# Kernel tuning notes

Measured on AMD Instinct MI355X. Metric: run time of the kernel, lower is better.

## Reference

```python
import jax, jax.numpy as jnp
import numpy as np

N_LAYERS = 3
N_HEADS = 8
N_HIDDEN = 16  # hidden_dim // n_heads
HIDDEN = 128
SLOPE = 0.2


def setup_inputs() -> dict:
    key = jax.random.key(0)
    ks = jax.random.split(key, 7)
    B, N, Din, Dh = 4, 512, 2, HIDDEN
    node_features = jax.random.normal(ks[0], (B, N, Din), dtype=jnp.float32)
    adj = jax.random.randint(ks[1], (B, N, N), 0, 2).astype(jnp.int32)
    adj = jnp.maximum(adj, jnp.eye(N, dtype=jnp.int32)[None])  # self loops -> no empty softmax rows
    s = 1.0 / np.sqrt(Dh)
    W_in = jax.random.normal(ks[2], (Din, Dh), dtype=jnp.float32) * (1.0 / np.sqrt(Din))
    W_l = jax.random.normal(ks[3], (N_LAYERS, Dh, N_HEADS * N_HIDDEN), dtype=jnp.float32) * s
    W_r = jax.random.normal(ks[4], (N_LAYERS, Dh, N_HEADS * N_HIDDEN), dtype=jnp.float32) * s
    attn_a = jax.random.normal(ks[5], (N_LAYERS, N_HIDDEN), dtype=jnp.float32) * (1.0 / np.sqrt(N_HIDDEN))
    W_out = jax.random.normal(ks[6], (Dh, 1), dtype=jnp.float32) * s
    return {"node_features": node_features, "adj": adj, "W_in": W_in,
            "W_l": W_l, "W_r": W_r, "attn_a": attn_a, "W_out": W_out}


def _gatv2_layer(h, adj, Wl, Wr, a):
    # h: [B,N,Dh]; adj: [B,N,N] int; Wl/Wr: [Dh, H*F]; a: [F]
    B, N, _ = h.shape
    g_l = (h @ Wl).reshape(B, N, N_HEADS, N_HIDDEN)
    g_r = (h @ Wr).reshape(B, N, N_HEADS, N_HIDDEN)
    # torch: g_sum[b,i,j] = g_l[b,j] + g_r[b,i]  (repeat vs repeat_interleave)
    g_sum = g_r[:, :, None, :, :] + g_l[:, None, :, :, :]  # [B,N,N,H,F]
    e = jnp.einsum('bijhf,f->bijh', jax.nn.leaky_relu(g_sum, SLOPE), a)  # [B,N,N,H]
    e = jnp.where(adj[..., None] == 0, -jnp.inf, e)
    att = jax.nn.softmax(e, axis=2)  # softmax over neighbors j
    out = jnp.einsum('bijh,bjhf->bihf', att, g_r)  # aggregate g_r (per source)
    return out.reshape(B, N, N_HEADS * N_HIDDEN)


def reference(node_features, adj, W_in, W_l, W_r, attn_a, W_out):
    h = node_features @ W_in  # [B,N,128]
    for i in range(N_LAYERS):
        h = _gatv2_layer(h, adj, W_l[i], W_r[i], attn_a[i])
    return h @ W_out  # [B,N,1]
```

## Files before the change

kernel.cpp:

```cpp
#include <hip/hip_runtime.h>
#include <cstdint>
#include <math.h>

#define NB 4
#define NN 512
#define DH 128
#define NHEADS 8
#define NHID 16
#define SLOPE 0.2f
#define ITILE 64
#define SENTINEL -1e30f

__global__ __launch_bounds__(256) void pack_adj_kernel(
    const int* __restrict__ adj, uint32_t* __restrict__ adjb)
{
    const int t   = threadIdx.x;
    const int row = blockIdx.x * 16 + (t >> 4);
    const int w   = t & 15;
    const int4* p = (const int4*)(adj + (size_t)row * NN + w * 32);
    uint32_t m = 0;
#pragma unroll
    for (int c = 0; c < 8; ++c) {
        const int4 v = p[c];
        m |= (v.x != 0 ? 1u : 0u) << (c * 4 + 0);
        m |= (v.y != 0 ? 1u : 0u) << (c * 4 + 1);
        m |= (v.z != 0 ? 1u : 0u) << (c * 4 + 2);
        m |= (v.w != 0 ? 1u : 0u) << (c * 4 + 3);
    }
    adjb[(size_t)row * 16 + w] = m;
}

__global__ __launch_bounds__(256) void proj_kernel(
    const float* __restrict__ h, const float* __restrict__ X,
    const float* __restrict__ Win,
    const float* __restrict__ Wl, const float* __restrict__ Wr,
    float* __restrict__ gl, float* __restrict__ gr)
{
    __shared__ __align__(16) float s_h[8][DH];
    const int bn0 = blockIdx.x * 8;
    const int b   = bn0 >> 9;
    const int n0  = bn0 & 511;
    const int t   = threadIdx.x;

    if (X) {
        if (t < DH) {
            const float w0 = Win[t], w1 = Win[DH + t];
#pragma unroll
            for (int r = 0; r < 8; ++r) {
                const float x0 = X[(bn0 + r) * 2 + 0];
                const float x1 = X[(bn0 + r) * 2 + 1];
                s_h[r][t] = x0 * w0 + x1 * w1;
            }
        }
    } else {
        for (int idx = t; idx < 8 * DH; idx += 256)
            s_h[idx >> 7][idx & 127] = h[(size_t)bn0 * DH + idx];
    }
    __syncthreads();

    const float* W = (t < DH) ? Wl : Wr;
    float*       g = (t < DH) ? gl : gr;
    const int f128 = t & 127;
    float acc[8] = {};
    for (int k = 0; k < DH; k += 4) {
        const float w0 = W[(k + 0) * DH + f128];
        const float w1 = W[(k + 1) * DH + f128];
        const float w2 = W[(k + 2) * DH + f128];
        const float w3 = W[(k + 3) * DH + f128];
#pragma unroll
        for (int r = 0; r < 8; ++r) {
            const float4 hv = *(const float4*)&s_h[r][k];
            acc[r] += hv.x * w0 + hv.y * w1 + hv.z * w2 + hv.w * w3;
        }
    }
    const int hh = f128 >> 4, f = f128 & 15;
    float* dst = g + ((size_t)(b * NHEADS + hh) * NN + n0) * NHID + f;
#pragma unroll
    for (int r = 0; r < 8; ++r)
        dst[r * NHID] = acc[r];
}

__global__ __launch_bounds__(512, 1) void attn_kernel(
    const float* __restrict__ gl, const float* __restrict__ gr,
    const uint32_t* __restrict__ adjb, const float* __restrict__ a_vec,
    float* __restrict__ h_out,
    const float* __restrict__ Wout, float* __restrict__ out)
{
    __shared__ __align__(16) float smem[19616];
    float* s_gl  = smem;
    float* s_gr  = smem + 8192;
    float* s_acc = smem;
    float* s_dgl = smem + 16384;
    float* s_dgr = smem + 16896;
    float* s_m   = smem + 17408;
    float* s_l   = smem + 18448;
    float* s_M   = smem + 19488;
    float* s_inv = smem + 19552;

    const int blk = blockIdx.x;
    const int it  = blk & 7;
    const int bh  = blk >> 3;
    const int b   = bh >> 3;
    const int hh  = bh & 7;
    const int i0  = it * ITILE;
    const int t   = threadIdx.x;
    const int il  = t & 31;
    const int js  = t >> 5;
    const int r0  = i0 + il;
    const int r1  = r0 + 32;

    const float4* pgl = (const float4*)(gl + (size_t)bh * NN * NHID);
    const float4* pgr = (const float4*)(gr + (size_t)bh * NN * NHID);
    float4 rl[4], rr[4];
#pragma unroll
    for (int k = 0; k < 4; ++k) { rl[k] = pgl[k * 512 + t]; rr[k] = pgr[k * 512 + t]; }

    const uint32_t mask0 = adjb[((size_t)(b * NN + r0)) * 16 + js];
    const uint32_t mask1 = adjb[((size_t)(b * NN + r1)) * 16 + js];

    float gri0[16], gri1[16];
#pragma unroll
    for (int q = 0; q < 4; ++q) {
        const float4 v0 = pgr[r0 * 4 + q];
        const float4 v1 = pgr[r1 * 4 + q];
        gri0[4*q+0] = v0.x; gri0[4*q+1] = v0.y; gri0[4*q+2] = v0.z; gri0[4*q+3] = v0.w;
        gri1[4*q+0] = v1.x; gri1[4*q+1] = v1.y; gri1[4*q+2] = v1.z; gri1[4*q+3] = v1.w;
    }

    float a[16];
#pragma unroll
    for (int q = 0; q < 4; ++q) {
        const float4 v = ((const float4*)a_vec)[q];
        a[4*q+0] = v.x; a[4*q+1] = v.y; a[4*q+2] = v.z; a[4*q+3] = v.w;
    }

    {
        float4* dl = (float4*)s_gl;
        float4* dr = (float4*)s_gr;
#pragma unroll
        for (int k = 0; k < 4; ++k) { dl[k * 512 + t] = rl[k]; dr[k * 512 + t] = rr[k]; }
    }

    {
        const float4 aq = ((const float4*)a_vec)[t & 3];
#pragma unroll
        for (int k = 0; k < 4; ++k) {
            float pl = rl[k].x * aq.x + rl[k].y * aq.y + rl[k].z * aq.z + rl[k].w * aq.w;
            float pr = rr[k].x * aq.x + rr[k].y * aq.y + rr[k].z * aq.z + rr[k].w * aq.w;
            pl += __shfl_xor(pl, 1); pl += __shfl_xor(pl, 2);
            pr += __shfl_xor(pr, 1); pr += __shfl_xor(pr, 2);
            if ((t & 3) == 0) {
                const int row = k * 128 + (t >> 2);
                s_dgl[row] = pl;
                s_dgr[row] = pr;
            }
        }
    }
    __syncthreads();

    const float c0 = 0.6f * s_dgr[r0];
    const float c1 = 0.6f * s_dgr[r1];
    const int jbase = js * 32;
    float sc0[32], sc1[32];
#pragma unroll
    for (int jj = 0; jj < 32; ++jj) {
        const int j = jbase + jj;
        const float4* pg = (const float4*)(s_gl + j * NHID);
        const float dj = s_dgl[j];
        float s0 = 0.f, s1 = 0.f;
#pragma unroll
        for (int q = 0; q < 4; ++q) {
            const float4 g = pg[q];
            float v;
            v = g.x + gri0[4*q+0]; s0 = fmaf(a[4*q+0], fabsf(v), s0);
            v = g.y + gri0[4*q+1]; s0 = fmaf(a[4*q+1], fabsf(v), s0);
            v = g.z + gri0[4*q+2]; s0 = fmaf(a[4*q+2], fabsf(v), s0);
            v = g.w + gri0[4*q+3]; s0 = fmaf(a[4*q+3], fabsf(v), s0);
            v = g.x + gri1[4*q+0]; s1 = fmaf(a[4*q+0], fabsf(v), s1);
            v = g.y + gri1[4*q+1]; s1 = fmaf(a[4*q+1], fabsf(v), s1);
            v = g.z + gri1[4*q+2]; s1 = fmaf(a[4*q+2], fabsf(v), s1);
            v = g.w + gri1[4*q+3]; s1 = fmaf(a[4*q+3], fabsf(v), s1);
        }
        const float b0 = fmaf(0.6f, dj, c0);
        const float b1 = fmaf(0.6f, dj, c1);
        sc0[jj] = ((mask0 >> jj) & 1u) ? fmaf(0.4f, s0, b0) : SENTINEL;
        sc1[jj] = ((mask1 >> jj) & 1u) ? fmaf(0.4f, s1, b1) : SENTINEL;
    }

    float m0 = sc0[0], m1 = sc1[0];
#pragma unroll
    for (int jj = 1; jj < 32; ++jj) { m0 = fmaxf(m0, sc0[jj]); m1 = fmaxf(m1, sc1[jj]); }
    float l0 = 0.f, l1 = 0.f;
#pragma unroll
    for (int jj = 0; jj < 32; ++jj) {
        sc0[jj] = __expf(sc0[jj] - m0); l0 += sc0[jj];
        sc1[jj] = __expf(sc1[jj] - m1); l1 += sc1[jj];
    }
    s_m[js * 65 + il]      = m0;
    s_m[js * 65 + il + 32] = m1;
    s_l[js * 65 + il]      = l0;
    s_l[js * 65 + il + 32] = l1;

    float acc0[16], acc1[16];
#pragma unroll
    for (int f = 0; f < 16; ++f) { acc0[f] = 0.f; acc1[f] = 0.f; }
#pragma unroll
    for (int jj = 0; jj < 32; ++jj) {
        const float4* pg = (const float4*)(s_gr + (jbase + jj) * NHID);
        const float p0 = sc0[jj], p1 = sc1[jj];
#pragma unroll
        for (int q = 0; q < 4; ++q) {
            const float4 g = pg[q];
            acc0[4*q+0] = fmaf(p0, g.x, acc0[4*q+0]);
            acc0[4*q+1] = fmaf(p0, g.y, acc0[4*q+1]);
            acc0[4*q+2] = fmaf(p0, g.z, acc0[4*q+2]);
            acc0[4*q+3] = fmaf(p0, g.w, acc0[4*q+3]);
            acc1[4*q+0] = fmaf(p1, g.x, acc1[4*q+0]);
            acc1[4*q+1] = fmaf(p1, g.y, acc1[4*q+1]);
            acc1[4*q+2] = fmaf(p1, g.z, acc1[4*q+2]);
            acc1[4*q+3] = fmaf(p1, g.w, acc1[4*q+3]);
        }
    }
    __syncthreads();

    if (t < 64) {
        float M = SENTINEL;
#pragma unroll
        for (int k = 0; k < 16; ++k) M = fmaxf(M, s_m[k * 65 + t]);
        float L = 0.f;
#pragma unroll
        for (int k = 0; k < 16; ++k) L += s_l[k * 65 + t] * __expf(s_m[k * 65 + t] - M);
        s_M[t]   = M;
        s_inv[t] = 1.f / L;
    }
    __syncthreads();

    {
        const float k0 = __expf(m0 - s_M[il])      * s_inv[il];
        const float k1 = __expf(m1 - s_M[il + 32]) * s_inv[il + 32];
        const int swz = il & 3;
        float* base_a = s_acc + js * 1024;
#pragma unroll
        for (int q = 0; q < 4; ++q) {
            float4 v0, v1;
            v0.x = acc0[4*q+0] * k0; v0.y = acc0[4*q+1] * k0;
            v0.z = acc0[4*q+2] * k0; v0.w = acc0[4*q+3] * k0;
            v1.x = acc1[4*q+0] * k1; v1.y = acc1[4*q+1] * k1;
            v1.z = acc1[4*q+2] * k1; v1.w = acc1[4*q+3] * k1;
            *(float4*)(base_a + il * 16        + 4 * (q ^ swz)) = v0;
            *(float4*)(base_a + (il + 32) * 16 + 4 * (q ^ swz)) = v1;
        }
    }
    __syncthreads();

    {
        const int i  = t >> 4;
        const int f  = t & 15;
        const int e  = f & 3, qf = f >> 2;
#pragma unroll
        for (int r = 0; r < 2; ++r) {
            const int lr = i + r * 32;
            const int w  = lr * 16 + 4 * (qf ^ (lr & 3)) + e;
            float o = 0.f;
#pragma unroll
            for (int k = 0; k < 16; ++k) o += s_acc[k * 1024 + w];
            const int grow = i0 + lr;
            if (Wout) {
                float v = o * Wout[hh * NHID + f];
#pragma unroll
                for (int off = 8; off; off >>= 1) v += __shfl_xor(v, off);
                if (f == 0) atomicAdd(out + b * NN + grow, v);
            } else {
                h_out[((size_t)(b * NN + grow)) * DH + hh * NHID + f] = o;
            }
        }
    }
}

extern "C" void kernel_launch(void* const* d_in, const int* in_sizes, int n_in,
                              void* d_out, int out_size, void* d_ws, size_t ws_size,
                              hipStream_t stream) {
    const float* X    = (const float*)d_in[0];
    const int*   adj  = (const int*)  d_in[1];
    const float* Win  = (const float*)d_in[2];
    const float* Wl   = (const float*)d_in[3];
    const float* Wr   = (const float*)d_in[4];
    const float* Aa   = (const float*)d_in[5];
    const float* Wout = (const float*)d_in[6];
    float* out = (float*)d_out;

    float*    ws   = (float*)d_ws;
    float*    h    = ws;
    float*    gl   = ws + 262144;
    float*    gr   = ws + 524288;
    uint32_t* adjb = (uint32_t*)(ws + 786432);

    pack_adj_kernel<<<NB * NN / 16, 256, 0, stream>>>(adj, adjb);
    hipMemsetAsync(out, 0, (size_t)out_size * sizeof(float), stream);

    for (int l = 0; l < 3; ++l) {
        proj_kernel<<<NB * NN / 8, 256, 0, stream>>>(
            h, (l == 0) ? X : nullptr, Win,
            Wl + (size_t)l * DH * DH, Wr + (size_t)l * DH * DH, gl, gr);
        const bool last = (l == 2);
        attn_kernel<<<NB * NHEADS * (NN / ITILE), 512, 0, stream>>>(
            gl, gr, adjb, Aa + l * NHID, h,
            last ? Wout : nullptr, out);
    }
}
```

Measured before the change: 163.0 us.

## Fuse projection, adjacency packing and memset into per-layer attention kernel

Merges the adjacency bit-packing, the input/weight projection and the output zeroing into a single per-layer attention kernel. Each block recomputes the per-head g_l/g_r projections for all 512 nodes straight into shared memory, so the separate projection kernel and its global round-trip go away. The launch count drops from eight to three. In exchange, every one of the 8 i-tile blocks per (batch, head) redundantly recomputes the same 512x16x2 projection. Shared memory use also grows, and the g arrays switch to a strided float4 layout.

New measurement: 170.5 us. +4.6%, slower.

```diff
diff --git a/kernel.cpp b/kernel.cpp
--- a/kernel.cpp
+++ b/kernel.cpp
@@ -7,95 +7,31 @@
 #define DH 128
 #define NHEADS 8
 #define NHID 16
-#define SLOPE 0.2f
 #define ITILE 64
 #define SENTINEL -1e30f
 
-__global__ __launch_bounds__(256) void pack_adj_kernel(
-    const int* __restrict__ adj, uint32_t* __restrict__ adjb)
+__global__ __launch_bounds__(512, 1) void gat_layer(
+    const int lay,
+    const float* __restrict__ X, const float* __restrict__ hin,
+    float* __restrict__ hout,
+    const float* __restrict__ Win,
+    const float* __restrict__ WlL, const float* __restrict__ WrL,
+    const float* __restrict__ a_vec, const float* __restrict__ Wout,
+    float* __restrict__ out, uint32_t* __restrict__ adjb,
+    const int* __restrict__ adj)
 {
-    const int t   = threadIdx.x;
-    const int row = blockIdx.x * 16 + (t >> 4);
-    const int w   = t & 15;
-    const int4* p = (const int4*)(adj + (size_t)row * NN + w * 32);
-    uint32_t m = 0;
-#pragma unroll
-    for (int c = 0; c < 8; ++c) {
-        const int4 v = p[c];
-        m |= (v.x != 0 ? 1u : 0u) << (c * 4 + 0);
-        m |= (v.y != 0 ? 1u : 0u) << (c * 4 + 1);
-        m |= (v.z != 0 ? 1u : 0u) << (c * 4 + 2);
-        m |= (v.w != 0 ? 1u : 0u) << (c * 4 + 3);
-    }
-    adjb[(size_t)row * 16 + w] = m;
-}
-
-__global__ __launch_bounds__(256) void proj_kernel(
-    const float* __restrict__ h, const float* __restrict__ X,
-    const float* __restrict__ Win,
-    const float* __restrict__ Wl, const float* __restrict__ Wr,
-    float* __restrict__ gl, float* __restrict__ gr)
-{
-    __shared__ __align__(16) float s_h[8][DH];
-    const int bn0 = blockIdx.x * 8;
-    const int b   = bn0 >> 9;
-    const int n0  = bn0 & 511;
-    const int t   = threadIdx.x;
-
-    if (X) {
-        if (t < DH) {
-            const float w0 = Win[t], w1 = Win[DH + t];
-#pragma unroll
-            for (int r = 0; r < 8; ++r) {
-                const float x0 = X[(bn0 + r) * 2 + 0];
-                const float x1 = X[(bn0 + r) * 2 + 1];
-                s_h[r][t] = x0 * w0 + x1 * w1;
-            }
-        }
-    } else {
-        for (int idx = t; idx < 8 * DH; idx += 256)
-            s_h[idx >> 7][idx & 127] = h[(size_t)bn0 * DH + idx];
-    }
-    __syncthreads();
-
-    const float* W = (t < DH) ? Wl : Wr;
-    float*       g = (t < DH) ? gl : gr;
-    const int f128 = t & 127;
-    float acc[8] = {};
-    for (int k = 0; k < DH; k += 4) {
-        const float w0 = W[(k + 0) * DH + f128];
-        const float w1 = W[(k + 1) * DH + f128];
-        const float w2 = W[(k + 2) * DH + f128];
-        const float w3 = W[(k + 3) * DH + f128];
-#pragma unroll
-        for (int r = 0; r < 8; ++r) {
-            const float4 hv = *(const float4*)&s_h[r][k];
-            acc[r] += hv.x * w0 + hv.y * w1 + hv.z * w2 + hv.w * w3;
-        }
-    }
-    const int hh = f128 >> 4, f = f128 & 15;
-    float* dst = g + ((size_t)(b * NHEADS + hh) * NN + n0) * NHID + f;
-#pragma unroll
-    for (int r = 0; r < 8; ++r)
-        dst[r * NHID] = acc[r];
-}
-
-__global__ __launch_bounds__(512, 1) void attn_kernel(
-    const float* __restrict__ gl, const float* __restrict__ gr,
-    const uint32_t* __restrict__ adjb, const float* __restrict__ a_vec,
-    float* __restrict__ h_out,
-    const float* __restrict__ Wout, float* __restrict__ out)
-{
-    __shared__ __align__(16) float smem[19616];
-    float* s_gl  = smem;
-    float* s_gr  = smem + 8192;
-    float* s_acc = smem;
-    float* s_dgl = smem + 16384;
-    float* s_dgr = smem + 16896;
-    float* s_m   = smem + 17408;
-    float* s_l   = smem + 18448;
-    float* s_M   = smem + 19488;
-    float* s_inv = smem + 19552;
+    __shared__ __align__(16) float smem[23968];
+    float* s_W   = smem;
+    float* s_acc = smem + 4096;
+    float* s_Win = smem + 20480;
+    float* s_dgl = smem + 20736;
+    float* s_dgr = smem + 21248;
+    float* s_m   = smem + 21760;
+    float* s_l   = smem + 22800;
+    float* s_M   = smem + 23840;
+    float* s_inv = smem + 23904;
+    float4* Sgl  = (float4*)(smem + 4096);
+    float4* Sgr  = (float4*)(smem + 12288);
 
     const int blk = blockIdx.x;
     const int it  = blk & 7;
@@ -109,22 +45,11 @@
     const int r0  = i0 + il;
     const int r1  = r0 + 32;
 
-    const float4* pgl = (const float4*)(gl + (size_t)bh * NN * NHID);
-    const float4* pgr = (const float4*)(gr + (size_t)bh * NN * NHID);
-    float4 rl[4], rr[4];
-#pragma unroll
-    for (int k = 0; k < 4; ++k) { rl[k] = pgl[k * 512 + t]; rr[k] = pgr[k * 512 + t]; }
-
-    const uint32_t mask0 = adjb[((size_t)(b * NN + r0)) * 16 + js];
-    const uint32_t mask1 = adjb[((size_t)(b * NN + r1)) * 16 + js];
-
-    float gri0[16], gri1[16];
-#pragma unroll
-    for (int q = 0; q < 4; ++q) {
-        const float4 v0 = pgr[r0 * 4 + q];
-        const float4 v1 = pgr[r1 * 4 + q];
-        gri0[4*q+0] = v0.x; gri0[4*q+1] = v0.y; gri0[4*q+2] = v0.z; gri0[4*q+3] = v0.w;
-        gri1[4*q+0] = v1.x; gri1[4*q+1] = v1.y; gri1[4*q+2] = v1.z; gri1[4*q+3] = v1.w;
+    {
+        const int sk = t >> 2, sq = (t & 3) * 4;
+        *(float4*)&s_W[sk * 32 + sq]      = *(const float4*)&WlL[sk * DH + hh * NHID + sq];
+        *(float4*)&s_W[sk * 32 + 16 + sq] = *(const float4*)&WrL[sk * DH + hh * NHID + sq];
+        if (lay == 0 && t < 64) ((float4*)s_Win)[t] = ((const float4*)Win)[t];
     }
 
     float a[16];
@@ -134,29 +59,106 @@
         a[4*q+0] = v.x; a[4*q+1] = v.y; a[4*q+2] = v.z; a[4*q+3] = v.w;
     }
 
-    {
-        float4* dl = (float4*)s_gl;
-        float4* dr = (float4*)s_gr;
-#pragma unroll
-        for (int k = 0; k < 4; ++k) { dl[k * 512 + t] = rl[k]; dr[k * 512 + t] = rr[k]; }
-    }
-
-    {
-        const float4 aq = ((const float4*)a_vec)[t & 3];
-#pragma unroll
-        for (int k = 0; k < 4; ++k) {
-            float pl = rl[k].x * aq.x + rl[k].y * aq.y + rl[k].z * aq.z + rl[k].w * aq.w;
-            float pr = rr[k].x * aq.x + rr[k].y * aq.y + rr[k].z * aq.z + rr[k].w * aq.w;
-            pl += __shfl_xor(pl, 1); pl += __shfl_xor(pl, 2);
-            pr += __shfl_xor(pr, 1); pr += __shfl_xor(pr, 2);
-            if ((t & 3) == 0) {
-                const int row = k * 128 + (t >> 2);
-                s_dgl[row] = pl;
-                s_dgr[row] = pr;
+    uint32_t mask0, mask1;
+    if (lay == 0) {
+        const int4* p0 = (const int4*)(adj + ((size_t)(b * NN + r0)) * NN + js * 32);
+        const int4* p1 = (const int4*)(adj + ((size_t)(b * NN + r1)) * NN + js * 32);
+        uint32_t m0 = 0, m1 = 0;
+#pragma unroll
+        for (int c = 0; c < 8; ++c) {
+            const int4 v0 = p0[c], v1 = p1[c];
+            m0 |= (v0.x != 0 ? 1u : 0u) << (c * 4 + 0);
+            m0 |= (v0.y != 0 ? 1u : 0u) << (c * 4 + 1);
+            m0 |= (v0.z != 0 ? 1u : 0u) << (c * 4 + 2);
+            m0 |= (v0.w != 0 ? 1u : 0u) << (c * 4 + 3);
+            m1 |= (v1.x != 0 ? 1u : 0u) << (c * 4 + 0);
+            m1 |= (v1.y != 0 ? 1u : 0u) << (c * 4 + 1);
+            m1 |= (v1.z != 0 ? 1u : 0u) << (c * 4 + 2);
+            m1 |= (v1.w != 0 ? 1u : 0u) << (c * 4 + 3);
+        }
+        mask0 = m0; mask1 = m1;
+        adjb[((size_t)(b * NN + r0)) * 16 + js] = m0;
+        adjb[((size_t)(b * NN + r1)) * 16 + js] = m1;
+    } else {
+        mask0 = adjb[((size_t)(b * NN + r0)) * 16 + js];
+        mask1 = adjb[((size_t)(b * NN + r1)) * 16 + js];
+    }
+    __syncthreads();
+
+    float4 agl[4], agr[4];
+#pragma unroll
+    for (int q = 0; q < 4; ++q) {
+        agl[q].x = 0.f; agl[q].y = 0.f; agl[q].z = 0.f; agl[q].w = 0.f;
+        agr[q].x = 0.f; agr[q].y = 0.f; agr[q].z = 0.f; agr[q].w = 0.f;
+    }
+    {
+        const float* hrow = (lay > 0) ? (hin + ((size_t)(b * NN + t)) * DH) : nullptr;
+        float x0 = 0.f, x1 = 0.f;
+        if (lay == 0) {
+            x0 = X[(b * NN + t) * 2 + 0];
+            x1 = X[(b * NN + t) * 2 + 1];
+        }
+#pragma unroll 2
+        for (int k = 0; k < DH; k += 4) {
+            float4 h4;
+            if (lay == 0) {
+                const float4 w0 = *(const float4*)&s_Win[k];
+                const float4 w1 = *(const float4*)&s_Win[DH + k];
+                h4.x = x0 * w0.x + x1 * w1.x;
+                h4.y = x0 * w0.y + x1 * w1.y;
+                h4.z = x0 * w0.z + x1 * w1.z;
+                h4.w = x0 * w0.w + x1 * w1.w;
+            } else {
+                h4 = *(const float4*)&hrow[k];
             }
-        }
-    }
-    __syncthreads();
+            const float* hp = &h4.x;
+#pragma unroll
+            for (int kk = 0; kk < 4; ++kk) {
+                const float hk = hp[kk];
+                const float* wrow = &s_W[(k + kk) * 32];
+#pragma unroll
+                for (int q = 0; q < 4; ++q) {
+                    const float4 wl = *(const float4*)&wrow[q * 4];
+                    const float4 wr = *(const float4*)&wrow[16 + q * 4];
+                    agl[q].x = fmaf(hk, wl.x, agl[q].x);
+                    agl[q].y = fmaf(hk, wl.y, agl[q].y);
+                    agl[q].z = fmaf(hk, wl.z, agl[q].z);
+                    agl[q].w = fmaf(hk, wl.w, agl[q].w);
+                    agr[q].x = fmaf(hk, wr.x, agr[q].x);
+                    agr[q].y = fmaf(hk, wr.y, agr[q].y);
+                    agr[q].z = fmaf(hk, wr.z, agr[q].z);
+                    agr[q].w = fmaf(hk, wr.w, agr[q].w);
+                }
+            }
+        }
+    }
+    {
+        float dl = 0.f, dr = 0.f;
+#pragma unroll
+        for (int q = 0; q < 4; ++q) {
+            dl = fmaf(a[4*q+0], agl[q].x, dl); dl = fmaf(a[4*q+1], agl[q].y, dl);
+            dl = fmaf(a[4*q+2], agl[q].z, dl); dl = fmaf(a[4*q+3], agl[q].w, dl);
+            dr = fmaf(a[4*q+0], agr[q].x, dr); dr = fmaf(a[4*q+1], agr[q].y, dr);
+            dr = fmaf(a[4*q+2], agr[q].z, dr); dr = fmaf(a[4*q+3], agr[q].w, dr);
+        }
+        s_dgl[t] = dl;
+        s_dgr[t] = dr;
+    }
+#pragma unroll
+    for (int q = 0; q < 4; ++q) {
+        Sgl[q * 512 + t] = agl[q];
+        Sgr[q * 512 + t] = agr[q];
+    }
+    __syncthreads();
+
+    float gri0[16], gri1[16];
+#pragma unroll
+    for (int q = 0; q < 4; ++q) {
+        const float4 v0 = Sgr[q * 512 + r0];
+        const float4 v1 = Sgr[q * 512 + r1];
+        gri0[4*q+0] = v0.x; gri0[4*q+1] = v0.y; gri0[4*q+2] = v0.z; gri0[4*q+3] = v0.w;
+        gri1[4*q+0] = v1.x; gri1[4*q+1] = v1.y; gri1[4*q+2] = v1.z; gri1[4*q+3] = v1.w;
+    }
 
     const float c0 = 0.6f * s_dgr[r0];
     const float c1 = 0.6f * s_dgr[r1];
@@ -165,12 +167,11 @@
 #pragma unroll
     for (int jj = 0; jj < 32; ++jj) {
         const int j = jbase + jj;
-        const float4* pg = (const float4*)(s_gl + j * NHID);
         const float dj = s_dgl[j];
         float s0 = 0.f, s1 = 0.f;
 #pragma unroll
         for (int q = 0; q < 4; ++q) {
-            const float4 g = pg[q];
+            const float4 g = Sgl[q * 512 + j];
             float v;
             v = g.x + gri0[4*q+0]; s0 = fmaf(a[4*q+0], fabsf(v), s0);
             v = g.y + gri0[4*q+1]; s0 = fmaf(a[4*q+1], fabsf(v), s0);
@@ -206,11 +207,11 @@
     for (int f = 0; f < 16; ++f) { acc0[f] = 0.f; acc1[f] = 0.f; }
 #pragma unroll
     for (int jj = 0; jj < 32; ++jj) {
-        const float4* pg = (const float4*)(s_gr + (jbase + jj) * NHID);
+        const int j = jbase + jj;
         const float p0 = sc0[jj], p1 = sc1[jj];
 #pragma unroll
         for (int q = 0; q < 4; ++q) {
-            const float4 g = pg[q];
+            const float4 g = Sgr[q * 512 + j];
             acc0[4*q+0] = fmaf(p0, g.x, acc0[4*q+0]);
             acc0[4*q+1] = fmaf(p0, g.y, acc0[4*q+1]);
             acc0[4*q+2] = fmaf(p0, g.z, acc0[4*q+2]);
@@ -271,10 +272,12 @@
                 for (int off = 8; off; off >>= 1) v += __shfl_xor(v, off);
                 if (f == 0) atomicAdd(out + b * NN + grow, v);
             } else {
-                h_out[((size_t)(b * NN + grow)) * DH + hh * NHID + f] = o;
+                hout[((size_t)(b * NN + grow)) * DH + hh * NHID + f] = o;
             }
         }
     }
+
+    if (lay == 1 && blk < 4) out[blk * 512 + t] = 0.f;
 }
 
 extern "C" void kernel_launch(void* const* d_in, const int* in_sizes, int n_in,
@@ -290,21 +293,14 @@
     float* out = (float*)d_out;
 
     float*    ws   = (float*)d_ws;
-    float*    h    = ws;
-    float*    gl   = ws + 262144;
-    float*    gr   = ws + 524288;
-    uint32_t* adjb = (uint32_t*)(ws + 786432);
-
-    pack_adj_kernel<<<NB * NN / 16, 256, 0, stream>>>(adj, adjb);
-    hipMemsetAsync(out, 0, (size_t)out_size * sizeof(float), stream);
-
-    for (int l = 0; l < 3; ++l) {
-        proj_kernel<<<NB * NN / 8, 256, 0, stream>>>(
-            h, (l == 0) ? X : nullptr, Win,
-            Wl + (size_t)l * DH * DH, Wr + (size_t)l * DH * DH, gl, gr);
-        const bool last = (l == 2);
-        attn_kernel<<<NB * NHEADS * (NN / ITILE), 512, 0, stream>>>(
-            gl, gr, adjb, Aa + l * NHID, h,
-            last ? Wout : nullptr, out);
-    }
+    float*    h_a  = ws;
+    float*    h_b  = ws + 262144;
+    uint32_t* adjb = (uint32_t*)(ws + 524288);
+
+    gat_layer<<<256, 512, 0, stream>>>(0, X, nullptr, h_a, Win,
+        Wl,              Wr,              Aa,      nullptr, out, adjb, adj);
+    gat_layer<<<256, 512, 0, stream>>>(1, nullptr, h_a, h_b, Win,
+        Wl + DH * DH,    Wr + DH * DH,    Aa + 16, nullptr, out, adjb, adj);
+    gat_layer<<<256, 512, 0, stream>>>(2, nullptr, h_b, nullptr, Win,
+        Wl + 2 * DH * DH, Wr + 2 * DH * DH, Aa + 32, Wout,  out, adjb, adj);
 }
```

## Double attention threads per block, fuse adjacency packing and output zeroing

Applied to the files above, without the earlier changes.

Each attention block now uses 1024 threads, each handling 16 neighbours instead of 32, and the two halves' partial softmax states are merged in shared memory. The adjacency bit-packing is folded into the first projection kernel, and zeroing of the output moves into the first attention kernel, which removes two launches. The score-add and aggregation FMAs are written with packed fp32 instructions via inline asm. This costs an extra merge stage and barriers, plus more shared memory.

Result: no change. 166.1 us (+1.9%).

```diff
diff --git a/kernel.cpp b/kernel.cpp
--- a/kernel.cpp
+++ b/kernel.cpp
@@ -7,34 +7,34 @@
 #define DH 128
 #define NHEADS 8
 #define NHID 16
-#define SLOPE 0.2f
 #define ITILE 64
 #define SENTINEL -1e30f
 
-__global__ __launch_bounds__(256) void pack_adj_kernel(
-    const int* __restrict__ adj, uint32_t* __restrict__ adjb)
-{
-    const int t   = threadIdx.x;
-    const int row = blockIdx.x * 16 + (t >> 4);
-    const int w   = t & 15;
-    const int4* p = (const int4*)(adj + (size_t)row * NN + w * 32);
-    uint32_t m = 0;
-#pragma unroll
-    for (int c = 0; c < 8; ++c) {
-        const int4 v = p[c];
-        m |= (v.x != 0 ? 1u : 0u) << (c * 4 + 0);
-        m |= (v.y != 0 ? 1u : 0u) << (c * 4 + 1);
-        m |= (v.z != 0 ? 1u : 0u) << (c * 4 + 2);
-        m |= (v.w != 0 ? 1u : 0u) << (c * 4 + 3);
-    }
-    adjb[(size_t)row * 16 + w] = m;
+typedef __attribute__((ext_vector_type(2))) float f32x2;
+__device__ __forceinline__ f32x2 pk_fma_blo(f32x2 a, f32x2 b, f32x2 c) {
+    f32x2 d;
+    asm("v_pk_fma_f32 %0, %1, %2, %3 op_sel_hi:[1,0,1]"
+        : "=v"(d) : "v"(a), "v"(b), "v"(c));
+    return d;
+}
+__device__ __forceinline__ f32x2 pk_fma_bhi(f32x2 a, f32x2 b, f32x2 c) {
+    f32x2 d;
+    asm("v_pk_fma_f32 %0, %1, %2, %3 op_sel:[0,1,0] op_sel_hi:[1,1,1]"
+        : "=v"(d) : "v"(a), "v"(b), "v"(c));
+    return d;
+}
+__device__ __forceinline__ f32x2 pk_add(f32x2 a, f32x2 b) {
+    f32x2 d;
+    asm("v_pk_add_f32 %0, %1, %2" : "=v"(d) : "v"(a), "v"(b));
+    return d;
 }
 
 __global__ __launch_bounds__(256) void proj_kernel(
     const float* __restrict__ h, const float* __restrict__ X,
     const float* __restrict__ Win,
     const float* __restrict__ Wl, const float* __restrict__ Wr,
-    float* __restrict__ gl, float* __restrict__ gr)
+    float* __restrict__ gl, float* __restrict__ gr,
+    const int* __restrict__ adj, uint32_t* __restrict__ adjb)
 {
     __shared__ __align__(16) float s_h[8][DH];
     const int bn0 = blockIdx.x * 8;
@@ -51,6 +51,21 @@
                 const float x1 = X[(bn0 + r) * 2 + 1];
                 s_h[r][t] = x0 * w0 + x1 * w1;
             }
+        }
+        if (t < 128) {
+            const int rg = bn0 + (t >> 4);
+            const int w  = t & 15;
+            const int4* p = (const int4*)(adj + (size_t)rg * NN + w * 32);
+            uint32_t m = 0;
+#pragma unroll
+            for (int c = 0; c < 8; ++c) {
+                const int4 v = p[c];
+                m |= (v.x != 0 ? 1u : 0u) << (c * 4 + 0);
+                m |= (v.y != 0 ? 1u : 0u) << (c * 4 + 1);
+                m |= (v.z != 0 ? 1u : 0u) << (c * 4 + 2);
+                m |= (v.w != 0 ? 1u : 0u) << (c * 4 + 3);
+            }
+            adjb[(size_t)rg * 16 + w] = m;
         }
     } else {
         for (int idx = t; idx < 8 * DH; idx += 256)
@@ -80,22 +95,23 @@
         dst[r * NHID] = acc[r];
 }
 
-__global__ __launch_bounds__(512, 1) void attn_kernel(
+__global__ __launch_bounds__(1024) void attn_kernel(
     const float* __restrict__ gl, const float* __restrict__ gr,
     const uint32_t* __restrict__ adjb, const float* __restrict__ a_vec,
     float* __restrict__ h_out,
-    const float* __restrict__ Wout, float* __restrict__ out)
+    const float* __restrict__ Wout, float* __restrict__ out,
+    const int zero_out)
 {
-    __shared__ __align__(16) float smem[19616];
+    __shared__ __align__(16) float smem[21696];
     float* s_gl  = smem;
     float* s_gr  = smem + 8192;
-    float* s_acc = smem;
+    float* scr   = smem;
     float* s_dgl = smem + 16384;
     float* s_dgr = smem + 16896;
     float* s_m   = smem + 17408;
-    float* s_l   = smem + 18448;
-    float* s_M   = smem + 19488;
-    float* s_inv = smem + 19552;
+    float* s_l   = smem + 19488;
+    float* s_M   = smem + 21568;
+    float* s_inv = smem + 21632;
 
     const int blk = blockIdx.x;
     const int it  = blk & 7;
@@ -108,23 +124,26 @@
     const int js  = t >> 5;
     const int r0  = i0 + il;
     const int r1  = r0 + 32;
+    const int jbase = js * 16;
 
     const float4* pgl = (const float4*)(gl + (size_t)bh * NN * NHID);
     const float4* pgr = (const float4*)(gr + (size_t)bh * NN * NHID);
-    float4 rl[4], rr[4];
-#pragma unroll
-    for (int k = 0; k < 4; ++k) { rl[k] = pgl[k * 512 + t]; rr[k] = pgr[k * 512 + t]; }
-
-    const uint32_t mask0 = adjb[((size_t)(b * NN + r0)) * 16 + js];
-    const uint32_t mask1 = adjb[((size_t)(b * NN + r1)) * 16 + js];
-
-    float gri0[16], gri1[16];
+    float4 rl[2], rr[2];
+#pragma unroll
+    for (int k = 0; k < 2; ++k) { rl[k] = pgl[k * 1024 + t]; rr[k] = pgr[k * 1024 + t]; }
+
+    const uint32_t wrd0 = adjb[((size_t)(b * NN + r0)) * 16 + (js >> 1)];
+    const uint32_t wrd1 = adjb[((size_t)(b * NN + r1)) * 16 + (js >> 1)];
+    const uint32_t mask0 = (wrd0 >> ((js & 1) * 16)) & 0xFFFFu;
+    const uint32_t mask1 = (wrd1 >> ((js & 1) * 16)) & 0xFFFFu;
+
+    f32x2 gri0p[8], gri1p[8];
 #pragma unroll
     for (int q = 0; q < 4; ++q) {
         const float4 v0 = pgr[r0 * 4 + q];
         const float4 v1 = pgr[r1 * 4 + q];
-        gri0[4*q+0] = v0.x; gri0[4*q+1] = v0.y; gri0[4*q+2] = v0.z; gri0[4*q+3] = v0.w;
-        gri1[4*q+0] = v1.x; gri1[4*q+1] = v1.y; gri1[4*q+2] = v1.z; gri1[4*q+3] = v1.w;
+        gri0p[2*q+0] = (f32x2){v0.x, v0.y}; gri0p[2*q+1] = (f32x2){v0.z, v0.w};
+        gri1p[2*q+0] = (f32x2){v1.x, v1.y}; gri1p[2*q+1] = (f32x2){v1.z, v1.w};
     }
 
     float a[16];
@@ -138,19 +157,18 @@
         float4* dl = (float4*)s_gl;
         float4* dr = (float4*)s_gr;
 #pragma unroll
-        for (int k = 0; k < 4; ++k) { dl[k * 512 + t] = rl[k]; dr[k * 512 + t] = rr[k]; }
-    }
-
+        for (int k = 0; k < 2; ++k) { dl[k * 1024 + t] = rl[k]; dr[k * 1024 + t] = rr[k]; }
+    }
     {
         const float4 aq = ((const float4*)a_vec)[t & 3];
 #pragma unroll
-        for (int k = 0; k < 4; ++k) {
+        for (int k = 0; k < 2; ++k) {
             float pl = rl[k].x * aq.x + rl[k].y * aq.y + rl[k].z * aq.z + rl[k].w * aq.w;
             float pr = rr[k].x * aq.x + rr[k].y * aq.y + rr[k].z * aq.z + rr[k].w * aq.w;
             pl += __shfl_xor(pl, 1); pl += __shfl_xor(pl, 2);
             pr += __shfl_xor(pr, 1); pr += __shfl_xor(pr, 2);
             if ((t & 3) == 0) {
-                const int row = k * 128 + (t >> 2);
+                const int row = k * 256 + (t >> 2);
                 s_dgl[row] = pl;
                 s_dgr[row] = pr;
             }
@@ -160,10 +178,9 @@
 
     const float c0 = 0.6f * s_dgr[r0];
     const float c1 = 0.6f * s_dgr[r1];
-    const int jbase = js * 32;
-    float sc0[32], sc1[32];
-#pragma unroll
-    for (int jj = 0; jj < 32; ++jj) {
+    float sc0[16], sc1[16];
+#pragma unroll
+    for (int jj = 0; jj < 16; ++jj) {
         const int j = jbase + jj;
         const float4* pg = (const float4*)(s_gl + j * NHID);
         const float dj = s_dgl[j];
@@ -171,15 +188,19 @@
 #pragma unroll
         for (int q = 0; q < 4; ++q) {
             const float4 g = pg[q];
-            float v;
-            v = g.x + gri0[4*q+0]; s0 = fmaf(a[4*q+0], fabsf(v), s0);
-            v = g.y + gri0[4*q+1]; s0 = fmaf(a[4*q+1], fabsf(v), s0);
-            v = g.z + gri0[4*q+2]; s0 = fmaf(a[4*q+2], fabsf(v), s0);
-            v = g.w + gri0[4*q+3]; s0 = fmaf(a[4*q+3], fabsf(v), s0);
-            v = g.x + gri1[4*q+0]; s1 = fmaf(a[4*q+0], fabsf(v), s1);
-            v = g.y + gri1[4*q+1]; s1 = fmaf(a[4*q+1], fabsf(v), s1);
-            v = g.z + gri1[4*q+2]; s1 = fmaf(a[4*q+2], fabsf(v), s1);
-            v = g.w + gri1[4*q+3]; s1 = fmaf(a[4*q+3], fabsf(v), s1);
+            const f32x2 Ga = {g.x, g.y}, Gb = {g.z, g.w};
+            const f32x2 v0a = pk_add(Ga, gri0p[2*q+0]);
+            const f32x2 v0b = pk_add(Gb, gri0p[2*q+1]);
+            const f32x2 v1a = pk_add(Ga, gri1p[2*q+0]);
+            const f32x2 v1b = pk_add(Gb, gri1p[2*q+1]);
+            s0 = fmaf(a[4*q+0], fabsf(v0a.x), s0);
+            s0 = fmaf(a[4*q+1], fabsf(v0a.y), s0);
+            s0 = fmaf(a[4*q+2], fabsf(v0b.x), s0);
+            s0 = fmaf(a[4*q+3], fabsf(v0b.y), s0);
+            s1 = fmaf(a[4*q+0], fabsf(v1a.x), s1);
+            s1 = fmaf(a[4*q+1], fabsf(v1a.y), s1);
+            s1 = fmaf(a[4*q+2], fabsf(v1b.x), s1);
+            s1 = fmaf(a[4*q+3], fabsf(v1b.y), s1);
         }
         const float b0 = fmaf(0.6f, dj, c0);
         const float b1 = fmaf(0.6f, dj, c1);
@@ -189,10 +210,10 @@
 
     float m0 = sc0[0], m1 = sc1[0];
 #pragma unroll
-    for (int jj = 1; jj < 32; ++jj) { m0 = fmaxf(m0, sc0[jj]); m1 = fmaxf(m1, sc1[jj]); }
+    for (int jj = 1; jj < 16; ++jj) { m0 = fmaxf(m0, sc0[jj]); m1 = fmaxf(m1, sc1[jj]); }
     float l0 = 0.f, l1 = 0.f;
 #pragma unroll
-    for (int jj = 0; jj < 32; ++jj) {
+    for (int jj = 0; jj < 16; ++jj) {
         sc0[jj] = __expf(sc0[jj] - m0); l0 += sc0[jj];
         sc1[jj] = __expf(sc1[jj] - m1); l1 += sc1[jj];
     }
@@ -201,25 +222,71 @@
     s_l[js * 65 + il]      = l0;
     s_l[js * 65 + il + 32] = l1;
 
-    float acc0[16], acc1[16];
-#pragma unroll
-    for (int f = 0; f < 16; ++f) { acc0[f] = 0.f; acc1[f] = 0.f; }
-#pragma unroll
-    for (int jj = 0; jj < 32; ++jj) {
-        const float4* pg = (const float4*)(s_gr + (jbase + jj) * NHID);
-        const float p0 = sc0[jj], p1 = sc1[jj];
+    f32x2 acc0p[8], acc1p[8];
+#pragma unroll
+    for (int f = 0; f < 8; ++f) { acc0p[f] = (f32x2){0.f, 0.f}; acc1p[f] = (f32x2){0.f, 0.f}; }
+#pragma unroll
+    for (int jj = 0; jj < 16; ++jj) {
+        const int j = jbase + jj;
+        const float4* pg = (const float4*)(s_gr + j * NHID);
+        const f32x2 pp = {sc0[jj], sc1[jj]};
 #pragma unroll
         for (int q = 0; q < 4; ++q) {
             const float4 g = pg[q];
-            acc0[4*q+0] = fmaf(p0, g.x, acc0[4*q+0]);
-            acc0[4*q+1] = fmaf(p0, g.y, acc0[4*q+1]);
-            acc0[4*q+2] = fmaf(p0, g.z, acc0[4*q+2]);
-            acc0[4*q+3] = fmaf(p0, g.w, acc0[4*q+3]);
-            acc1[4*q+0] = fmaf(p1, g.x, acc1[4*q+0]);
-            acc1[4*q+1] = fmaf(p1, g.y, acc1[4*q+1]);
-            acc1[4*q+2] = fmaf(p1, g.z, acc1[4*q+2]);
-            acc1[4*q+3] = fmaf(p1, g.w, acc1[4*q+3]);
-        }
+            const f32x2 Ga = {g.x, g.y}, Gb = {g.z, g.w};
+            acc0p[2*q+0] = pk_fma_blo(Ga, pp, acc0p[2*q+0]);
+            acc0p[2*q+1] = pk_fma_blo(Gb, pp, acc0p[2*q+1]);
+            acc1p[2*q+0] = pk_fma_bhi(Ga, pp, acc1p[2*q+0]);
+            acc1p[2*q+1] = pk_fma_bhi(Gb, pp, acc1p[2*q+1]);
+        }
+    }
+    __syncthreads();
+
+    const int swz = il & 3;
+    if (js >= 16) {
+        float* basep = scr + (js - 16) * 1024;
+#pragma unroll
+        for (int q = 0; q < 4; ++q) {
+            float4 v0, v1;
+            v0.x = acc0p[2*q+0].x; v0.y = acc0p[2*q+0].y;
+            v0.z = acc0p[2*q+1].x; v0.w = acc0p[2*q+1].y;
+            v1.x = acc1p[2*q+0].x; v1.y = acc1p[2*q+0].y;
+            v1.z = acc1p[2*q+1].x; v1.w = acc1p[2*q+1].y;
+            *(float4*)(basep + il * 16        + 4 * (q ^ swz)) = v0;
+            *(float4*)(basep + (il + 32) * 16 + 4 * (q ^ swz)) = v1;
+        }
+    }
+    __syncthreads();
+
+    if (js < 16) {
+        const float pm0 = s_m[(js + 16) * 65 + il];
+        const float pm1 = s_m[(js + 16) * 65 + il + 32];
+        const float pl0 = s_l[(js + 16) * 65 + il];
+        const float pl1 = s_l[(js + 16) * 65 + il + 32];
+        const float nm0 = fmaxf(m0, pm0), nm1 = fmaxf(m1, pm1);
+        const float wa0 = __expf(m0 - nm0), wb0 = __expf(pm0 - nm0);
+        const float wa1 = __expf(m1 - nm1), wb1 = __expf(pm1 - nm1);
+        l0 = l0 * wa0 + pl0 * wb0;
+        l1 = l1 * wa1 + pl1 * wb1;
+        float* basep = scr + js * 1024;
+#pragma unroll
+        for (int q = 0; q < 4; ++q) {
+            const float4 o0 = *(const float4*)(basep + il * 16        + 4 * (q ^ swz));
+            const float4 o1 = *(const float4*)(basep + (il + 32) * 16 + 4 * (q ^ swz));
+            acc0p[2*q+0].x = acc0p[2*q+0].x * wa0 + o0.x * wb0;
+            acc0p[2*q+0].y = acc0p[2*q+0].y * wa0 + o0.y * wb0;
+            acc0p[2*q+1].x = acc0p[2*q+1].x * wa0 + o0.z * wb0;
+            acc0p[2*q+1].y = acc0p[2*q+1].y * wa0 + o0.w * wb0;
+            acc1p[2*q+0].x = acc1p[2*q+0].x * wa1 + o1.x * wb1;
+            acc1p[2*q+0].y = acc1p[2*q+0].y * wa1 + o1.y * wb1;
+            acc1p[2*q+1].x = acc1p[2*q+1].x * wa1 + o1.z * wb1;
+            acc1p[2*q+1].y = acc1p[2*q+1].y * wa1 + o1.w * wb1;
+        }
+        m0 = nm0; m1 = nm1;
+        s_m[js * 65 + il]      = m0;
+        s_m[js * 65 + il + 32] = m1;
+        s_l[js * 65 + il]      = l0;
+        s_l[js * 65 + il + 32] = l1;
     }
     __syncthreads();
 
@@ -235,20 +302,19 @@
     }
     __syncthreads();
 
-    {
+    if (js < 16) {
         const float k0 = __expf(m0 - s_M[il])      * s_inv[il];
         const float k1 = __expf(m1 - s_M[il + 32]) * s_inv[il + 32];
-        const int swz = il & 3;
-        float* base_a = s_acc + js * 1024;
+        float* basep = scr + js * 1024;
 #pragma unroll
         for (int q = 0; q < 4; ++q) {
             float4 v0, v1;
-            v0.x = acc0[4*q+0] * k0; v0.y = acc0[4*q+1] * k0;
-            v0.z = acc0[4*q+2] * k0; v0.w = acc0[4*q+3] * k0;
-            v1.x = acc1[4*q+0] * k1; v1.y = acc1[4*q+1] * k1;
-            v1.z = acc1[4*q+2] * k1; v1.w = acc1[4*q+3] * k1;
-            *(float4*)(base_a + il * 16        + 4 * (q ^ swz)) = v0;
-            *(float4*)(base_a + (il + 32) * 16 + 4 * (q ^ swz)) = v1;
+            v0.x = acc0p[2*q+0].x * k0; v0.y = acc0p[2*q+0].y * k0;
+            v0.z = acc0p[2*q+1].x * k0; v0.w = acc0p[2*q+1].y * k0;
+            v1.x = acc1p[2*q+0].x * k1; v1.y = acc1p[2*q+0].y * k1;
+            v1.z = acc1p[2*q+1].x * k1; v1.w = acc1p[2*q+1].y * k1;
+            *(float4*)(basep + il * 16        + 4 * (q ^ swz)) = v0;
+            *(float4*)(basep + (il + 32) * 16 + 4 * (q ^ swz)) = v1;
         }
     }
     __syncthreads();
@@ -257,24 +323,22 @@
         const int i  = t >> 4;
         const int f  = t & 15;
         const int e  = f & 3, qf = f >> 2;
-#pragma unroll
-        for (int r = 0; r < 2; ++r) {
-            const int lr = i + r * 32;
-            const int w  = lr * 16 + 4 * (qf ^ (lr & 3)) + e;
-            float o = 0.f;
-#pragma unroll
-            for (int k = 0; k < 16; ++k) o += s_acc[k * 1024 + w];
-            const int grow = i0 + lr;
-            if (Wout) {
-                float v = o * Wout[hh * NHID + f];
-#pragma unroll
-                for (int off = 8; off; off >>= 1) v += __shfl_xor(v, off);
-                if (f == 0) atomicAdd(out + b * NN + grow, v);
-            } else {
-                h_out[((size_t)(b * NN + grow)) * DH + hh * NHID + f] = o;
-            }
-        }
-    }
+        const int w  = i * 16 + 4 * (qf ^ (i & 3)) + e;
+        float o = 0.f;
+#pragma unroll
+        for (int k = 0; k < 16; ++k) o += scr[k * 1024 + w];
+        const int grow = i0 + i;
+        if (Wout) {
+            float v = o * Wout[hh * NHID + f];
+#pragma unroll
+            for (int off = 8; off; off >>= 1) v += __shfl_xor(v, off);
+            if (f == 0) atomicAdd(out + b * NN + grow, v);
+        } else {
+            h_out[((size_t)(b * NN + grow)) * DH + hh * NHID + f] = o;
+        }
+    }
+
+    if (zero_out && blk < 2) out[blk * 1024 + t] = 0.f;
 }
 
 extern "C" void kernel_launch(void* const* d_in, const int* in_sizes, int n_in,
@@ -290,21 +354,24 @@
     float* out = (float*)d_out;
 
     float*    ws   = (float*)d_ws;
-    float*    h    = ws;
-    float*    gl   = ws + 262144;
-    float*    gr   = ws + 524288;
-    uint32_t* adjb = (uint32_t*)(ws + 786432);
-
-    pack_adj_kernel<<<NB * NN / 16, 256, 0, stream>>>(adj, adjb);
-    hipMemsetAsync(out, 0, (size_t)out_size * sizeof(float), stream);
-
-    for (int l = 0; l < 3; ++l) {
-        proj_kernel<<<NB * NN / 8, 256, 0, stream>>>(
-            h, (l == 0) ? X : nullptr, Win,
-            Wl + (size_t)l * DH * DH, Wr + (size_t)l * DH * DH, gl, gr);
-        const bool last = (l == 2);
-        attn_kernel<<<NB * NHEADS * (NN / ITILE), 512, 0, stream>>>(
-            gl, gr, adjb, Aa + l * NHID, h,
-            last ? Wout : nullptr, out);
-    }
-}
+    float*    h_a  = ws;
+    float*    h_b  = ws + 262144;
+    float*    gl   = ws + 524288;
+    float*    gr   = ws + 786432;
+    uint32_t* adjb = (uint32_t*)(ws + 1048576);
+
+    proj_kernel<<<NB * NN / 8, 256, 0, stream>>>(
+        nullptr, X, Win, Wl, Wr, gl, gr, adj, adjb);
+    attn_kernel<<<NB * NHEADS * (NN / ITILE), 1024, 0, stream>>>(
+        gl, gr, adjb, Aa, h_a, nullptr, out, 1);
+
+    proj_kernel<<<NB * NN / 8, 256, 0, stream>>>(
+        h_a, nullptr, Win, Wl + DH * DH, Wr + DH * DH, gl, gr, adj, adjb);
+    attn_kernel<<<NB * NHEADS * (NN / ITILE), 1024, 0, stream>>>(
+        gl, gr, adjb, Aa + NHID, h_b, nullptr, out, 0);
+
+    proj_kernel<<<NB * NN / 8, 256, 0, stream>>>(
+        h_b, nullptr, Win, Wl + 2 * DH * DH, Wr + 2 * DH * DH, gl, gr, adj, adjb);
+    attn_kernel<<<NB * NHEADS * (NN / ITILE), 1024, 0, stream>>>(
+        gl, gr, adjb, Aa + 2 * NHID, nullptr, Wout, out, 0);
+}
```
